# Performance work log

Measured on AMD Instinct MI355X. Metric: run time of the kernel, lower is better.

Reference implementation:

```python
import jax, jax.numpy as jnp
import numpy as np

B, OBS, ACT = 16384, 39, 4
D = 400            # backbone_hidden[-1] == expert_hidden[-1] == task_queries_dim
NE, NT = 8, 10     # num_experts, num_tasks


def setup_inputs() -> dict:
    key = jax.random.key(0)
    ks = jax.random.split(key, 20)
    g = lambda k, shp, fan: jax.random.normal(k, shp, dtype=jnp.float32) / np.sqrt(fan)
    return {
        "obs": jax.random.normal(ks[0], (B, OBS), dtype=jnp.float32),
        "act": jax.random.normal(ks[1], (B, ACT), dtype=jnp.float32),
        "task": jax.random.randint(ks[2], (B,), 0, NT),
        # backbone mlp: [obs+act, 400, 400], relu after each layer
        "bb_w1": g(ks[3], (OBS + ACT, D), OBS + ACT), "bb_b1": jnp.zeros((D,), jnp.float32),
        "bb_w2": g(ks[4], (D, D), D), "bb_b2": jnp.zeros((D,), jnp.float32),
        # 8 expert mlps, stacked: [400 -> 400 -> 400], relu after each layer
        "ex_w1": g(ks[5], (NE, D, D), D), "ex_b1": jnp.zeros((NE, D), jnp.float32),
        "ex_w2": g(ks[6], (NE, D, D), D), "ex_b2": jnp.zeros((NE, D), jnp.float32),
        # attention params
        "key_mat": g(ks[7], (NE, D, D), D),
        "value_mat": g(ks[8], (NE, D, D), D),
        "task_queries": jax.random.normal(ks[9], (NT, D), dtype=jnp.float32),
        # tower mlp: [400, 400, 400, 1], relu on hidden layers, identity output
        "tw_w1": g(ks[10], (D, D), D), "tw_b1": jnp.zeros((D,), jnp.float32),
        "tw_w2": g(ks[11], (D, D), D), "tw_b2": jnp.zeros((D,), jnp.float32),
        "tw_w3": g(ks[12], (D, 1), D), "tw_b3": jnp.zeros((1,), jnp.float32),
    }


def reference(obs, act, task, bb_w1, bb_b1, bb_w2, bb_b2,
              ex_w1, ex_b1, ex_w2, ex_b2,
              key_mat, value_mat, task_queries,
              tw_w1, tw_b1, tw_w2, tw_b2, tw_w3, tw_b3):
    x = jnp.concatenate([obs, act], axis=-1)                       # [B, obs+act]
    h = jax.nn.relu(x @ bb_w1 + bb_b1)
    h = jax.nn.relu(h @ bb_w2 + bb_b2)                             # [B, D]
    # all experts as one batched GEMM: e[n, b, :] = expert_n(h[b])
    e = jax.nn.relu(jnp.einsum('bi,nij->nbj', h, ex_w1) + ex_b1[:, None, :])
    e = jax.nn.relu(jnp.einsum('nbi,nij->nbj', e, ex_w2) + ex_b2[:, None, :])  # [NE, B, D]
    # per-expert key/value projections (einsum 'nij,nj->ni' batched over b)
    vals = jnp.einsum('nij,nbj->bni', value_mat, e)                # [B, NE, D]
    keys = jnp.einsum('nij,nbj->bni', key_mat, e)                  # [B, NE, D]
    q = task_queries[task]                                         # [B, D]
    scores = jnp.einsum('bni,bi->bn', keys, q)                     # [B, NE]
    w = jax.nn.softmax(scores, axis=-1)                            # softmax over experts
    tower_in = jnp.einsum('bn,bni->bi', w, vals)                   # [B, D]
    t = jax.nn.relu(tower_in @ tw_w1 + tw_b1)
    t = jax.nn.relu(t @ tw_w2 + tw_b2)
    qval = t @ tw_w3 + tw_b3                                       # [B, 1]
    return jnp.squeeze(qval, -1)                                   # [B]
```

## Files before the change

kernel.cpp:

```cpp
#include <hip/hip_runtime.h>

typedef _Float16 f16;
typedef f16 f16x8 __attribute__((ext_vector_type(8)));
typedef float f32x4 __attribute__((ext_vector_type(4)));

#define NB 16384
#define D 400
#define DP 416
#define NEXP 8
#define NTASK 10
#define NKT 13

#define MEMFENCE asm volatile("" ::: "memory")
#define BAR() do{ MEMFENCE; __builtin_amdgcn_s_barrier(); MEMFENCE; }while(0)
#define VM(N) asm volatile("s_waitcnt vmcnt(" #N ")" ::: "memory")
#define LGKM0 asm volatile("s_waitcnt lgkmcnt(0)" ::: "memory")

static __device__ __forceinline__ f32x4 mfma16x32(f16x8 a, f16x8 b, f32x4 c){
  return __builtin_amdgcn_mfma_f32_16x16x32_f16(a, b, c, 0, 0, 0);
}
static __device__ __forceinline__ void g2l(const void* g, void* l){
  __builtin_amdgcn_global_load_lds((const __attribute__((address_space(1))) void*)g,
      (__attribute__((address_space(3))) void*)l, 16, 0, 0);
}
static __device__ __forceinline__ f16x8 scale8(f16x8 a, f16 s){
  f16x8 r;
  #pragma unroll
  for (int e=0;e<8;e++) r[e] = a[e]*s;
  return r;
}

static __device__ __forceinline__ void stage_duo(const char* wbase, char* lds, int kt,
                                                 int t0, int dd, int h, int lane){
  const int r = lane >> 3, c = lane & 7, cg = c ^ r;
  g2l(wbase + (size_t)((t0 + dd*2 + (cg>>2))*16 + h*8 + r)*832 + (size_t)kt*64 + (cg&3)*16,
      lds + dd*2048 + h*1024);
}
static __device__ __forceinline__ f16x8 rdB(const f16* buf, int dloc, int t, int lhi, int l15){
  return *(const f16x8*)(buf + dloc*1024 + l15*64 + ((((t*4+lhi) ^ (l15&7)))<<3));
}
static __device__ __forceinline__ f16x8 rdL(const f16* lact, int r, int kt, int lhi){
  int q = kt*4 + lhi;
  int c = (q < 48) ? (q ^ (r&7)) : q;
  return *(const f16x8*)(lact + r*416 + (c<<3));
}
static __device__ __forceinline__ int lact_idx(int r, int col){
  int q = col >> 3;
  int c = (q < 48) ? (q ^ (r&7)) : q;
  return r*416 + (c<<3) + (col&7);
}
static __device__ __forceinline__ void stageB4(const char* wb, char* buf, int kt,
                                               int wv, int lane){
  for (int u = wv; u < 26; u += 4) stage_duo(wb, buf, kt, 0, u>>1, u&1, lane);
}


__global__ void k_build_x(const float* __restrict__ obs, const float* __restrict__ act,
                          f16* __restrict__ x)
{
  int idx = blockIdx.x*256 + threadIdx.x;
  int b = idx >> 6, c = idx & 63;
  float v = 0.f;
  if (c < 39) v = obs[b*39 + c];
  else if (c < 43) v = act[b*4 + (c - 39)];
  x[idx] = (f16)v;
}

__global__ void k_transpose_all(
    const float* __restrict__ bb_w1, const float* __restrict__ bb_w2,
    const float* __restrict__ ex_w1, const float* __restrict__ ex_w2,
    const float* __restrict__ tw_w1, const float* __restrict__ tw_w2,
    f16* __restrict__ bbw1T, f16* __restrict__ bbw2T,
    f16* __restrict__ exw1T, f16* __restrict__ exw2T,
    f16* __restrict__ tw1T,  f16* __restrict__ tw2T)
{
  __shared__ float t[32][33];
  const int z = blockIdx.z;
  const float* in; f16* out; int K = D;
  if (z == 0){ in = bb_w1; out = bbw1T; K = 43; }
  else if (z == 1){ in = bb_w2; out = bbw2T; }
  else if (z < 10){ in = ex_w1 + (size_t)(z-2)*D*D;  out = exw1T + (size_t)(z-2)*DP*DP; }
  else if (z < 18){ in = ex_w2 + (size_t)(z-10)*D*D; out = exw2T + (size_t)(z-10)*DP*DP; }
  else if (z == 18){ in = tw_w1; out = tw1T; }
  else { in = tw_w2; out = tw2T; }
  int tx = threadIdx.x & 31, ty = threadIdx.x >> 5;
  int n0 = blockIdx.x*32, k0 = blockIdx.y*32;
  #pragma unroll
  for (int r=0;r<4;r++){
    int k = k0 + ty + r*8, nn = n0 + tx;
    t[ty + r*8][tx] = (k < K && nn < D) ? in[(size_t)k*D + nn] : 0.f;
  }
  __syncthreads();
  #pragma unroll
  for (int r=0;r<4;r++){
    int nn = n0 + ty + r*8, kp = k0 + tx;
    if (nn < DP && kp < DP) out[(size_t)nn*DP + kp] = (f16)t[tx][ty + r*8];
  }
}

__global__ void k_val_pad(const float* __restrict__ in, f16* __restrict__ out)
{
  int idx = blockIdx.x*256 + threadIdx.x;
  if (idx >= NEXP*DP*DP) return;
  int c = idx % DP, r = (idx / DP) % DP, n = idx / (DP*DP);
  float v = (r < D && c < D) ? in[((size_t)n*D + r)*D + c] : 0.f;
  out[idx] = (f16)v;
}

__global__ void k_kq(const float* __restrict__ key_mat, const float* __restrict__ tq,
                     float* __restrict__ kq)
{
  __shared__ float tqs[NTASK*D];
  int n = blockIdx.x, tid = threadIdx.x;
  for (int i=tid;i<NTASK*D;i+=256) tqs[i] = tq[i];
  __syncthreads();
  float a0[NTASK], a1[NTASK];
  #pragma unroll
  for (int t=0;t<NTASK;t++){ a0[t]=0.f; a1[t]=0.f; }
  const float* km = key_mat + (size_t)n*D*D;
  for (int i=0;i<D;i++){
    float v0 = km[(size_t)i*D + tid];
    float v1 = (tid+256 < D) ? km[(size_t)i*D + tid + 256] : 0.f;
    #pragma unroll
    for (int t=0;t<NTASK;t++){
      float q = tqs[t*D + i];
      a0[t] += v0*q; a1[t] += v1*q;
    }
  }
  #pragma unroll
  for (int t=0;t<NTASK;t++){
    kq[(size_t)n*NTASK*DP + t*DP + tid] = a0[t];
    if (tid+256 < DP) kq[(size_t)n*NTASK*DP + t*DP + tid+256] = (tid+256 < D) ? a1[t] : 0.f;
  }
}


#define MFMA26(a0_, a1_, BUF) do {                                              \
    __builtin_amdgcn_s_setprio(1);                                              \
    _Pragma("unroll")                                                           \
    for (int j=0;j<13;j++){                                                     \
      int tj = ch*13 + j;                                                       \
      f16x8 b = rdB((BUF), tj>>1, tj&1, lhi, l15);                              \
      acc[0][j] = mfma16x32((a0_), b, acc[0][j]);                               \
      acc[1][j] = mfma16x32((a1_), b, acc[1][j]);                               \
    }                                                                           \
    __builtin_amdgcn_s_setprio(0);                                              \
  } while(0)

#define MFMA13(a0_, BUF) do {                                                   \
    __builtin_amdgcn_s_setprio(1);                                              \
    _Pragma("unroll")                                                           \
    for (int j=0;j<13;j++){                                                     \
      int tj = ch*13 + j;                                                       \
      f16x8 b = rdB((BUF), tj>>1, tj&1, lhi, l15);                              \
      acc[j] = mfma16x32((a0_), b, acc[j]);                                     \
    }                                                                           \
    __builtin_amdgcn_s_setprio(0);                                              \
  } while(0)

#define STAGE_W(wb_, buf_, p_, full_) do{                                       \
    int tot_ = (full_) ? 52 : 26;                                               \
    for (int u = wv; u < tot_; u += 4){                                         \
      int kh_ = (u >= 26) ? 1 : 0, uu_ = u - (kh_ ? 26 : 0);                    \
      stage_duo((wb_), (char*)(buf_)[kh_], 2*(p_)+kh_, 0, uu_>>1, uu_&1, lane); \
    }                                                                           \
  } while(0)

__global__ __launch_bounds__(256,2) void k_experts(
    const f16* __restrict__ h16, const f16* __restrict__ w1T, const float* __restrict__ b1s,
    const f16* __restrict__ w2T, const float* __restrict__ b2s,
    f16* __restrict__ e16, const float* __restrict__ kqg, const int* __restrict__ task,
    float* __restrict__ scores)
{
  __shared__ f16 bufB[13*1024];
  __shared__ f16 lact[64*416];
  float (*psum)[2] = (float(*)[2])lact;
  const int tid = threadIdx.x, lane = tid & 63, wv = tid >> 6;
  const int l15 = lane & 15, lhi = lane >> 4;
  const int rh = wv >> 1, ch = wv & 1;
  const int n = blockIdx.x;
  const int rowbase = blockIdx.y * 64;
  const f32x4 Z4 = {0,0,0,0};
  f32x4 acc[2][13];

  const char* wb1 = (const char*)(w1T + (size_t)n*DP*DP);
  const char* wb2 = (const char*)(w2T + (size_t)n*DP*DP);
  const f16* Ab = h16 + (size_t)(rowbase + rh*32 + l15)*DP;

  #pragma unroll
  for (int j=0;j<13;j++){ acc[0][j]=Z4; acc[1][j]=Z4; }
  f16x8 a0 = *(const f16x8*)(Ab + lhi*8);
  f16x8 a1 = *(const f16x8*)(Ab + 16*DP + lhi*8);
  stageB4(wb1, (char*)bufB, 0, wv, lane);
  for (int kt=0; kt<NKT; kt++){
    VM(0); BAR();
    MFMA26(a0, a1, bufB);
    BAR();
    if (kt < NKT-1){
      a0 = *(const f16x8*)(Ab + (kt+1)*32 + lhi*8);
      a1 = *(const f16x8*)(Ab + 16*DP + (kt+1)*32 + lhi*8);
      stageB4(wb1, (char*)bufB, kt+1, wv, lane);
    }
  }
  stageB4(wb2, (char*)bufB, 0, wv, lane);
  #pragma unroll
  for (int j=0;j<13;j++){
    int col = (ch*13+j)*16 + l15;
    float bv = (col<D)? b1s[n*D+col] : 0.f;
    #pragma unroll
    for (int ar=0;ar<2;ar++)
      #pragma unroll
      for (int rr=0;rr<4;rr++){
        float v = acc[ar][j][rr] + bv; v = v>0.f?v:0.f;
        lact[lact_idx(rh*32+ar*16+lhi*4+rr, col)] = (f16)v;
      }
  }
  LGKM0;

  #pragma unroll
  for (int j=0;j<13;j++){ acc[0][j]=Z4; acc[1][j]=Z4; }
  for (int kt=0; kt<NKT; kt++){
    VM(0); BAR();
    f16x8 x0 = rdL(lact, rh*32 + l15, kt, lhi);
    f16x8 x1 = rdL(lact, rh*32 + 16 + l15, kt, lhi);
    MFMA26(x0, x1, bufB);
    BAR();
    if (kt < NKT-1) stageB4(wb2, (char*)bufB, kt+1, wv, lane);
  }
  const float* kqp[2][4];
  const float* kqb = kqg + (size_t)n*NTASK*DP;
  #pragma unroll
  for (int ar=0;ar<2;ar++)
    #pragma unroll
    for (int rr=0;rr<4;rr++){
      int grow = rowbase + rh*32 + ar*16 + lhi*4 + rr;
      kqp[ar][rr] = kqb + (size_t)task[grow]*DP;
    }
  float p_[2][4] = {{0,0,0,0},{0,0,0,0}};
  #pragma unroll
  for (int j=0;j<13;j++){
    int col = (ch*13+j)*16 + l15;
    float bv = (col<D)? b2s[n*D+col] : 0.f;
    #pragma unroll
    for (int ar=0;ar<2;ar++)
      #pragma unroll
      for (int rr=0;rr<4;rr++){
        float v = acc[ar][j][rr] + bv; v = v>0.f?v:0.f;
        e16[((size_t)n*NB + rowbase + rh*32+ar*16+lhi*4+rr)*DP + col] = (f16)v;
        p_[ar][rr] += v * kqp[ar][rr][col];
      }
  }
  #pragma unroll
  for (int ar=0;ar<2;ar++)
    #pragma unroll
    for (int rr=0;rr<4;rr++){
      float p = p_[ar][rr];
      p += __shfl_xor(p, 1, 64);
      p += __shfl_xor(p, 2, 64);
      p += __shfl_xor(p, 4, 64);
      p += __shfl_xor(p, 8, 64);
      if (l15 == 0) psum[rh*32+ar*16+lhi*4+rr][ch] = p;
    }
  LGKM0; BAR();
  if (tid < 64) scores[(size_t)(rowbase + tid)*NEXP + n] = psum[tid][0] + psum[tid][1];
}

__global__ __launch_bounds__(256,2) void k_backbone(
    const f16* __restrict__ x, const f16* __restrict__ w1T, const float* __restrict__ b1,
    const f16* __restrict__ w2T, const float* __restrict__ b2, f16* __restrict__ h16)
{
  __shared__ f16 bufB[2][13*1024];
  __shared__ f16 lact[32*416];
  const int tid = threadIdx.x, lane = tid & 63, wv = tid >> 6;
  const int l15 = lane & 15, lhi = lane >> 4;
  const int rh = wv >> 1, ch = wv & 1;
  const int rowbase = blockIdx.x * 32;
  const f32x4 Z4 = {0,0,0,0};
  f32x4 acc[13];

  const f16* Ab = x + (size_t)(rowbase + rh*16 + l15)*64;

  #pragma unroll
  for (int j=0;j<13;j++) acc[j]=Z4;
  STAGE_W((const char*)w1T, bufB, 0, 1);
  f16x8 a0 = *(const f16x8*)(Ab + lhi*8);
  f16x8 a1 = *(const f16x8*)(Ab + 32 + lhi*8);
  VM(0); BAR();
  MFMA13(a0, bufB[0]);
  MFMA13(a1, bufB[1]);
  BAR();
  STAGE_W((const char*)w2T, bufB, 0, 1);
  #pragma unroll
  for (int j=0;j<13;j++){
    int col = (ch*13+j)*16 + l15;
    float bv = (col<D)? b1[col] : 0.f;
    #pragma unroll
    for (int rr=0;rr<4;rr++){
      float v = acc[j][rr] + bv; v = v>0.f?v:0.f;
      lact[lact_idx(rh*16+lhi*4+rr, col)] = (f16)v;
    }
  }
  LGKM0;

  #pragma unroll
  for (int j=0;j<13;j++) acc[j]=Z4;
  for (int p=0; p<7; p++){
    VM(0); BAR();
    f16x8 x0 = rdL(lact, rh*16 + l15, 2*p, lhi);
    MFMA13(x0, bufB[0]);
    if (p < 6){
      f16x8 x1 = rdL(lact, rh*16 + l15, 2*p+1, lhi);
      MFMA13(x1, bufB[1]);
    }
    BAR();
    if (p < 6) STAGE_W((const char*)w2T, bufB, p+1, (p+1)<6);
  }
  #pragma unroll
  for (int j=0;j<13;j++){
    int col = (ch*13+j)*16 + l15;
    float bv = (col<D)? b2[col] : 0.f;
    #pragma unroll
    for (int rr=0;rr<4;rr++){
      float v = acc[j][rr] + bv; v = v>0.f?v:0.f;
      h16[(size_t)(rowbase + rh*16+lhi*4+rr)*DP + col] = (f16)v;
    }
  }
}

__global__ __launch_bounds__(256,2) void k_attn(
    const f16* __restrict__ e16, const f16* __restrict__ valT,
    const float* __restrict__ scores, f16* __restrict__ ti16)
{
  __shared__ f16 buf[2][7*1024];
  __shared__ float wsm[64*NEXP];
  const int tid = threadIdx.x, lane = tid & 63, wv = tid >> 6;
  const int l15 = lane & 15, lhi = lane >> 4;
  const int rg = wv >> 1, cg = wv & 1;
  const int cb = blockIdx.x;
  const int rowbase = blockIdx.y * 64;
  const int nd = cb ? 6 : 7;
  const int ntw = cb ? 6 : 7;
  const int t0 = cb * 14;
  const f32x4 Z4 = {0,0,0,0};
  f32x4 acc[2][7];
  #pragma unroll
  for (int a=0;a<2;a++)
    #pragma unroll
    for (int j=0;j<7;j++) acc[a][j]=Z4;

  if (tid < 64){
    const float* sr = scores + (size_t)(rowbase + tid)*NEXP;
    float s[8]; float m = -1e30f;
    #pragma unroll
    for (int k=0;k<8;k++){ s[k]=sr[k]; m = fmaxf(m, s[k]); }
    float sum = 0.f;
    #pragma unroll
    for (int k=0;k<8;k++){ s[k] = expf(s[k]-m); sum += s[k]; }
    float inv = 1.f/sum;
    #pragma unroll
    for (int k=0;k<8;k++) wsm[tid*NEXP + k] = s[k]*inv;
  }

  #define STAGE_A(n_, p_) do {                                                  \
    const char* vb_ = (const char*)(valT + (size_t)(n_)*DP*DP);                 \
    int nu_ = nd*2, tot_ = ((p_)<6) ? nd*4 : nd*2;                              \
    for (int u = wv; u < tot_; u += 4){                                         \
      int kh_ = (u >= nu_) ? 1 : 0, uu_ = u - (kh_ ? nu_ : 0);                  \
      stage_duo(vb_, (char*)buf[kh_], 2*(p_)+kh_, t0, uu_>>1, uu_&1, lane);     \
    }                                                                           \
  } while(0)

  #define LDA_A(n_, kt_, ar_) \
    (*(const f16x8*)(e16 + ((size_t)(n_)*NB + rowbase + rg*32 + (ar_)*16 + l15)*DP + (kt_)*32 + lhi*8))

  STAGE_A(0, 0);
  f16x8 aC00 = LDA_A(0,0,0), aC01 = LDA_A(0,0,1);
  f16x8 aC10 = LDA_A(0,1,0), aC11 = LDA_A(0,1,1);
  LGKM0;

  for (int n=0;n<NEXP;n++){
    for (int p=0;p<7;p++){
      int s = n*7 + p;
      VM(0); BAR();
      f16 w0 = (f16)wsm[(rg*32      + l15)*NEXP + n];
      f16 w1 = (f16)wsm[(rg*32 + 16 + l15)*NEXP + n];
      {
        f16x8 as0 = scale8(aC00, w0), as1 = scale8(aC01, w1);
        __builtin_amdgcn_s_setprio(1);
        #pragma unroll
        for (int j=0;j<7;j++) if (j<ntw){
          int tl = cg*ntw + j;
          f16x8 b = rdB(buf[0], tl>>1, tl&1, lhi, l15);
          acc[0][j] = mfma16x32(as0, b, acc[0][j]);
          acc[1][j] = mfma16x32(as1, b, acc[1][j]);
        }
        __builtin_amdgcn_s_setprio(0);
      }
      if (p < 6){
        f16x8 as0 = scale8(aC10, w0), as1 = scale8(aC11, w1);
        __builtin_amdgcn_s_setprio(1);
        #pragma unroll
        for (int j=0;j<7;j++) if (j<ntw){
          int tl = cg*ntw + j;
          f16x8 b = rdB(buf[1], tl>>1, tl&1, lhi, l15);
          acc[0][j] = mfma16x32(as0, b, acc[0][j]);
          acc[1][j] = mfma16x32(as1, b, acc[1][j]);
        }
        __builtin_amdgcn_s_setprio(0);
      }
      BAR();
      if (s < NEXP*7 - 1){
        int p2 = (p==6) ? 0 : p+1;
        int n2 = (p==6) ? n+1 : n;
        STAGE_A(n2, p2);
        aC00 = LDA_A(n2, 2*p2,   0); aC01 = LDA_A(n2, 2*p2,   1);
        if (p2 < 6){ aC10 = LDA_A(n2, 2*p2+1, 0); aC11 = LDA_A(n2, 2*p2+1, 1); }
      }
    }
  }
  #pragma unroll
  for (int ar=0;ar<2;ar++)
    #pragma unroll
    for (int j=0;j<7;j++) if (j<ntw){
      int col = (t0 + cg*ntw + j)*16 + l15;
      #pragma unroll
      for (int rr=0;rr<4;rr++)
        ti16[(size_t)(rowbase + rg*32 + ar*16 + lhi*4 + rr)*DP + col] = (f16)acc[ar][j][rr];
    }
}

__global__ __launch_bounds__(256,2) void k_mlp3(
    const f16* __restrict__ ti16,
    const f16* __restrict__ tw1T, const float* __restrict__ tb1,
    const f16* __restrict__ tw2T, const float* __restrict__ tb2,
    const float* __restrict__ tw3, const float* __restrict__ tb3,
    float* __restrict__ out)
{
  __shared__ f16 bufB[2][13*1024];
  __shared__ f16 lact[32*416];
  float (*psum)[2] = (float(*)[2])lact;
  const int tid = threadIdx.x, lane = tid & 63, wv = tid >> 6;
  const int l15 = lane & 15, lhi = lane >> 4;
  const int rh = wv >> 1, ch = wv & 1;
  const int rowbase = blockIdx.x * 32;
  const f32x4 Z4 = {0,0,0,0};
  f32x4 acc[13];

  const f16* Ab = ti16 + (size_t)(rowbase + rh*16 + l15)*DP;

  #pragma unroll
  for (int j=0;j<13;j++) acc[j]=Z4;
  STAGE_W((const char*)tw1T, bufB, 0, 1);
  f16x8 a0 = *(const f16x8*)(Ab + lhi*8);
  f16x8 a1 = *(const f16x8*)(Ab + 32 + lhi*8);
  for (int p=0; p<7; p++){
    VM(0); BAR();
    MFMA13(a0, bufB[0]);
    if (p < 6) MFMA13(a1, bufB[1]);
    BAR();
    if (p < 6){
      STAGE_W((const char*)tw1T, bufB, p+1, (p+1)<6);
      a0 = *(const f16x8*)(Ab + (2*p+2)*32 + lhi*8);
      if (p+1 < 6) a1 = *(const f16x8*)(Ab + (2*p+3)*32 + lhi*8);
    }
  }
  STAGE_W((const char*)tw2T, bufB, 0, 1);
  #pragma unroll
  for (int j=0;j<13;j++){
    int col = (ch*13+j)*16 + l15;
    float bv = (col<D)? tb1[col] : 0.f;
    #pragma unroll
    for (int rr=0;rr<4;rr++){
      float v = acc[j][rr] + bv; v = v>0.f?v:0.f;
      lact[lact_idx(rh*16+lhi*4+rr, col)] = (f16)v;
    }
  }
  LGKM0;

  #pragma unroll
  for (int j=0;j<13;j++) acc[j]=Z4;
  for (int p=0; p<7; p++){
    VM(0); BAR();
    f16x8 x0 = rdL(lact, rh*16 + l15, 2*p, lhi);
    MFMA13(x0, bufB[0]);
    if (p < 6){
      f16x8 x1 = rdL(lact, rh*16 + l15, 2*p+1, lhi);
      MFMA13(x1, bufB[1]);
    }
    BAR();
    if (p < 6) STAGE_W((const char*)tw2T, bufB, p+1, (p+1)<6);
  }
  float p_[4] = {0,0,0,0};
  #pragma unroll
  for (int j=0;j<13;j++){
    int col = (ch*13+j)*16 + l15;
    float bv = (col<D)? tb2[col] : 0.f;
    float w3 = (col<D)? tw3[col] : 0.f;
    #pragma unroll
    for (int rr=0;rr<4;rr++){
      float v = acc[j][rr] + bv; v = v>0.f?v:0.f;
      p_[rr] += v * w3;
    }
  }
  #pragma unroll
  for (int rr=0;rr<4;rr++){
    float p = p_[rr];
    p += __shfl_xor(p, 1, 64);
    p += __shfl_xor(p, 2, 64);
    p += __shfl_xor(p, 4, 64);
    p += __shfl_xor(p, 8, 64);
    if (l15 == 0) psum[rh*16+lhi*4+rr][ch] = p;
  }
  LGKM0; BAR();
  if (tid < 32) out[rowbase + tid] = psum[tid][0] + psum[tid][1] + tb3[0];
}


extern "C" void kernel_launch(void* const* d_in, const int* in_sizes, int n_in,
                              void* d_out, int out_size, void* d_ws, size_t ws_size,
                              hipStream_t stream)
{
  const float* obs     = (const float*)d_in[0];
  const float* act     = (const float*)d_in[1];
  const int*   task    = (const int*)  d_in[2];
  const float* bb_w1   = (const float*)d_in[3];
  const float* bb_b1   = (const float*)d_in[4];
  const float* bb_w2   = (const float*)d_in[5];
  const float* bb_b2   = (const float*)d_in[6];
  const float* ex_w1   = (const float*)d_in[7];
  const float* ex_b1   = (const float*)d_in[8];
  const float* ex_w2   = (const float*)d_in[9];
  const float* ex_b2   = (const float*)d_in[10];
  const float* key_mat = (const float*)d_in[11];
  const float* val_mat = (const float*)d_in[12];
  const float* tq      = (const float*)d_in[13];
  const float* tw_w1   = (const float*)d_in[14];
  const float* tw_b1   = (const float*)d_in[15];
  const float* tw_w2   = (const float*)d_in[16];
  const float* tw_b2   = (const float*)d_in[17];
  const float* tw_w3   = (const float*)d_in[18];
  const float* tw_b3   = (const float*)d_in[19];

  char* ws = (char*)d_ws;
  size_t off = 0;
  auto alloc = [&](size_t bytes){ void* p = ws + off; off += (bytes + 255) & ~(size_t)255; return p; };
  f16*   x16   = (f16*)  alloc((size_t)NB*64*2);
  f16*   h16   = (f16*)  alloc((size_t)NB*DP*2);
  f16*   e16   = (f16*)  alloc((size_t)NEXP*NB*DP*2);
  f16*   ti16  = (f16*)  alloc((size_t)NB*DP*2);
  float* scors = (float*)alloc((size_t)NB*NEXP*4);
  float* kq    = (float*)alloc((size_t)NEXP*NTASK*DP*4);
  f16*   bbw1T = (f16*)  alloc((size_t)DP*DP*2);
  f16*   bbw2T = (f16*)  alloc((size_t)DP*DP*2);
  f16*   exw1T = (f16*)  alloc((size_t)NEXP*DP*DP*2);
  f16*   exw2T = (f16*)  alloc((size_t)NEXP*DP*DP*2);
  f16*   valT  = (f16*)  alloc((size_t)NEXP*DP*DP*2);
  f16*   tw1T  = (f16*)  alloc((size_t)DP*DP*2);
  f16*   tw2T  = (f16*)  alloc((size_t)DP*DP*2);
  (void)ws_size; (void)in_sizes; (void)n_in; (void)out_size;

  k_build_x<<<NB*64/256, 256, 0, stream>>>(obs, act, x16);
  k_transpose_all<<<dim3(13,13,20), 256, 0, stream>>>(
      bb_w1, bb_w2, ex_w1, ex_w2, tw_w1, tw_w2,
      bbw1T, bbw2T, exw1T, exw2T, tw1T, tw2T);
  k_val_pad<<<(NEXP*DP*DP + 255)/256, 256, 0, stream>>>(val_mat, valT);
  k_kq<<<NEXP, 256, 0, stream>>>(key_mat, tq, kq);

  k_backbone<<<NB/32, 256, 0, stream>>>(x16, bbw1T, bb_b1, bbw2T, bb_b2, h16);
  k_experts<<<dim3(NEXP, NB/64), 256, 0, stream>>>(h16, exw1T, ex_b1, exw2T, ex_b2,
                                                   e16, kq, task, scors);
  k_attn<<<dim3(2, NB/64), 256, 0, stream>>>(e16, valT, scors, ti16);
  k_mlp3<<<NB/32, 256, 0, stream>>>(ti16, tw1T, tw_b1, tw2T, tw_b2, tw_w3, tw_b3,
                                    (float*)d_out);
}
```

Measured before the change: 400.5 us.

## Enlarge expert kernel tile to 128 rows with 512 threads and two k-steps per barrier

```diff
diff --git a/kernel.cpp b/kernel.cpp
--- a/kernel.cpp
+++ b/kernel.cpp
@@ -48,10 +48,6 @@
   int q = col >> 3;
   int c = (q < 48) ? (q ^ (r&7)) : q;
   return r*416 + (c<<3) + (col&7);
-}
-static __device__ __forceinline__ void stageB4(const char* wb, char* buf, int kt,
-                                               int wv, int lane){
-  for (int u = wv; u < 26; u += 4) stage_duo(wb, buf, kt, 0, u>>1, u&1, lane);
 }
 
 
@@ -166,20 +162,28 @@
     }                                                                           \
   } while(0)
 
-__global__ __launch_bounds__(256,2) void k_experts(
+#define STAGE_W8(wb_, buf_, p_, full_) do{                                      \
+    int tot_ = (full_) ? 52 : 26;                                               \
+    for (int u = wv; u < tot_; u += 8){                                         \
+      int kh_ = (u >= 26) ? 1 : 0, uu_ = u - (kh_ ? 26 : 0);                    \
+      stage_duo((wb_), (char*)(buf_)[kh_], 2*(p_)+kh_, 0, uu_>>1, uu_&1, lane); \
+    }                                                                           \
+  } while(0)
+
+__global__ __launch_bounds__(512,2) void k_experts(
     const f16* __restrict__ h16, const f16* __restrict__ w1T, const float* __restrict__ b1s,
     const f16* __restrict__ w2T, const float* __restrict__ b2s,
     f16* __restrict__ e16, const float* __restrict__ kqg, const int* __restrict__ task,
     float* __restrict__ scores)
 {
-  __shared__ f16 bufB[13*1024];
-  __shared__ f16 lact[64*416];
+  __shared__ f16 bufB[2][13*1024];
+  __shared__ f16 lact[128*416];
   float (*psum)[2] = (float(*)[2])lact;
   const int tid = threadIdx.x, lane = tid & 63, wv = tid >> 6;
   const int l15 = lane & 15, lhi = lane >> 4;
   const int rh = wv >> 1, ch = wv & 1;
   const int n = blockIdx.x;
-  const int rowbase = blockIdx.y * 64;
+  const int rowbase = blockIdx.y * 128;
   const f32x4 Z4 = {0,0,0,0};
   f32x4 acc[2][13];
 
@@ -189,20 +193,27 @@
 
   #pragma unroll
   for (int j=0;j<13;j++){ acc[0][j]=Z4; acc[1][j]=Z4; }
-  f16x8 a0 = *(const f16x8*)(Ab + lhi*8);
-  f16x8 a1 = *(const f16x8*)(Ab + 16*DP + lhi*8);
-  stageB4(wb1, (char*)bufB, 0, wv, lane);
-  for (int kt=0; kt<NKT; kt++){
+  STAGE_W8(wb1, bufB, 0, 1);
+  f16x8 a00 = *(const f16x8*)(Ab + lhi*8);
+  f16x8 a01 = *(const f16x8*)(Ab + 16*DP + lhi*8);
+  f16x8 a10 = *(const f16x8*)(Ab + 32 + lhi*8);
+  f16x8 a11 = *(const f16x8*)(Ab + 16*DP + 32 + lhi*8);
+  for (int p=0; p<7; p++){
     VM(0); BAR();
-    MFMA26(a0, a1, bufB);
+    MFMA26(a00, a01, bufB[0]);
+    if (p < 6) MFMA26(a10, a11, bufB[1]);
     BAR();
-    if (kt < NKT-1){
-      a0 = *(const f16x8*)(Ab + (kt+1)*32 + lhi*8);
-      a1 = *(const f16x8*)(Ab + 16*DP + (kt+1)*32 + lhi*8);
-      stageB4(wb1, (char*)bufB, kt+1, wv, lane);
-    }
-  }
-  stageB4(wb2, (char*)bufB, 0, wv, lane);
+    if (p < 6){
+      STAGE_W8(wb1, bufB, p+1, (p+1)<6);
+      a00 = *(const f16x8*)(Ab + (2*p+2)*32 + lhi*8);
+      a01 = *(const f16x8*)(Ab + 16*DP + (2*p+2)*32 + lhi*8);
+      if (p+1 < 6){
+        a10 = *(const f16x8*)(Ab + (2*p+3)*32 + lhi*8);
+        a11 = *(const f16x8*)(Ab + 16*DP + (2*p+3)*32 + lhi*8);
+      }
+    }
+  }
+  STAGE_W8(wb2, bufB, 0, 1);
   #pragma unroll
   for (int j=0;j<13;j++){
     int col = (ch*13+j)*16 + l15;
@@ -219,13 +230,20 @@
 
   #pragma unroll
   for (int j=0;j<13;j++){ acc[0][j]=Z4; acc[1][j]=Z4; }
-  for (int kt=0; kt<NKT; kt++){
+  for (int p=0; p<7; p++){
     VM(0); BAR();
-    f16x8 x0 = rdL(lact, rh*32 + l15, kt, lhi);
-    f16x8 x1 = rdL(lact, rh*32 + 16 + l15, kt, lhi);
-    MFMA26(x0, x1, bufB);
+    {
+      f16x8 x0 = rdL(lact, rh*32 + l15, 2*p, lhi);
+      f16x8 x1 = rdL(lact, rh*32 + 16 + l15, 2*p, lhi);
+      MFMA26(x0, x1, bufB[0]);
+    }
+    if (p < 6){
+      f16x8 x0 = rdL(lact, rh*32 + l15, 2*p+1, lhi);
+      f16x8 x1 = rdL(lact, rh*32 + 16 + l15, 2*p+1, lhi);
+      MFMA26(x0, x1, bufB[1]);
+    }
     BAR();
-    if (kt < NKT-1) stageB4(wb2, (char*)bufB, kt+1, wv, lane);
+    if (p < 6) STAGE_W8(wb2, bufB, p+1, (p+1)<6);
   }
   const float* kqp[2][4];
   const float* kqb = kqg + (size_t)n*NTASK*DP;
@@ -262,7 +280,7 @@
       if (l15 == 0) psum[rh*32+ar*16+lhi*4+rr][ch] = p;
     }
   LGKM0; BAR();
-  if (tid < 64) scores[(size_t)(rowbase + tid)*NEXP + n] = psum[tid][0] + psum[tid][1];
+  if (tid < 128) scores[(size_t)(rowbase + tid)*NEXP + n] = psum[tid][0] + psum[tid][1];
 }
 
 __global__ __launch_bounds__(256,2) void k_backbone(
@@ -567,8 +585,8 @@
   k_kq<<<NEXP, 256, 0, stream>>>(key_mat, tq, kq);
 
   k_backbone<<<NB/32, 256, 0, stream>>>(x16, bbw1T, bb_b1, bbw2T, bb_b2, h16);
-  k_experts<<<dim3(NEXP, NB/64), 256, 0, stream>>>(h16, exw1T, ex_b1, exw2T, ex_b2,
-                                                   e16, kq, task, scors);
+  k_experts<<<dim3(NEXP, NB/128), 512, 0, stream>>>(h16, exw1T, ex_b1, exw2T, ex_b2,
+                                                    e16, kq, task, scors);
   k_attn<<<dim3(2, NB/64), 256, 0, stream>>>(e16, valT, scors, ti16);
   k_mlp3<<<NB/32, 256, 0, stream>>>(ti16, tw1T, tw_b1, tw2T, tw_b2, tw_w3, tw_b3,
                                     (float*)d_out);
```

Result: no change. 407.1 us (+1.7%).

## Spill expert hidden layer to global memory and parallelize key-query precompute

Applied to the files above, without the earlier changes.

```diff
diff --git a/kernel.cpp b/kernel.cpp
--- a/kernel.cpp
+++ b/kernel.cpp
@@ -110,27 +110,28 @@
 __global__ void k_kq(const float* __restrict__ key_mat, const float* __restrict__ tq,
                      float* __restrict__ kq)
 {
+  __shared__ float kcol[D*32];
   __shared__ float tqs[NTASK*D];
-  int n = blockIdx.x, tid = threadIdx.x;
-  for (int i=tid;i<NTASK*D;i+=256) tqs[i] = tq[i];
+  const int n = blockIdx.x, cb = blockIdx.y, tid = threadIdx.x;
+  const int c0 = cb*32;
+  const float* km = key_mat + (size_t)n*D*D;
+  for (int idx=tid; idx<NTASK*D; idx+=256) tqs[idx] = tq[idx];
+  for (int idx=tid; idx<D*32; idx+=256){
+    int i = idx>>5, c = idx&31;
+    int col = c0 + c;
+    kcol[idx] = (col < D) ? km[(size_t)i*D + col] : 0.f;
+  }
   __syncthreads();
-  float a0[NTASK], a1[NTASK];
-  #pragma unroll
-  for (int t=0;t<NTASK;t++){ a0[t]=0.f; a1[t]=0.f; }
-  const float* km = key_mat + (size_t)n*D*D;
-  for (int i=0;i<D;i++){
-    float v0 = km[(size_t)i*D + tid];
-    float v1 = (tid+256 < D) ? km[(size_t)i*D + tid + 256] : 0.f;
-    #pragma unroll
-    for (int t=0;t<NTASK;t++){
-      float q = tqs[t*D + i];
-      a0[t] += v0*q; a1[t] += v1*q;
-    }
-  }
-  #pragma unroll
-  for (int t=0;t<NTASK;t++){
-    kq[(size_t)n*NTASK*DP + t*DP + tid] = a0[t];
-    if (tid+256 < DP) kq[(size_t)n*NTASK*DP + t*DP + tid+256] = (tid+256 < D) ? a1[t] : 0.f;
+  const int c = tid & 31, tg = tid >> 5;
+  #pragma unroll
+  for (int rep=0; rep<2; rep++){
+    int t = tg + rep*8;
+    if (t < NTASK){
+      float acc = 0.f;
+      for (int i=0;i<D;i++) acc += kcol[i*32+c] * tqs[t*D+i];
+      int col = c0 + c;
+      if (col < DP) kq[((size_t)n*NTASK + t)*DP + col] = acc;
+    }
   }
 }
 
@@ -166,15 +167,14 @@
     }                                                                           \
   } while(0)
 
-__global__ __launch_bounds__(256,2) void k_experts(
+__global__ __launch_bounds__(256,4) void k_experts(
     const f16* __restrict__ h16, const f16* __restrict__ w1T, const float* __restrict__ b1s,
     const f16* __restrict__ w2T, const float* __restrict__ b2s,
     f16* __restrict__ e16, const float* __restrict__ kqg, const int* __restrict__ task,
     float* __restrict__ scores)
 {
   __shared__ f16 bufB[13*1024];
-  __shared__ f16 lact[64*416];
-  float (*psum)[2] = (float(*)[2])lact;
+  __shared__ float psum[64][2];
   const int tid = threadIdx.x, lane = tid & 63, wv = tid >> 6;
   const int l15 = lane & 15, lhi = lane >> 4;
   const int rh = wv >> 1, ch = wv & 1;
@@ -185,20 +185,22 @@
 
   const char* wb1 = (const char*)(w1T + (size_t)n*DP*DP);
   const char* wb2 = (const char*)(w2T + (size_t)n*DP*DP);
-  const f16* Ab = h16 + (size_t)(rowbase + rh*32 + l15)*DP;
+  const f16* Ab1 = h16 + (size_t)(rowbase + rh*32 + l15)*DP;
+  f16* Eb = e16 + ((size_t)n*NB + rowbase)*DP;
+  const f16* Ab2 = Eb + (size_t)(rh*32 + l15)*DP;
 
   #pragma unroll
   for (int j=0;j<13;j++){ acc[0][j]=Z4; acc[1][j]=Z4; }
-  f16x8 a0 = *(const f16x8*)(Ab + lhi*8);
-  f16x8 a1 = *(const f16x8*)(Ab + 16*DP + lhi*8);
+  f16x8 a0 = *(const f16x8*)(Ab1 + lhi*8);
+  f16x8 a1 = *(const f16x8*)(Ab1 + 16*DP + lhi*8);
   stageB4(wb1, (char*)bufB, 0, wv, lane);
   for (int kt=0; kt<NKT; kt++){
     VM(0); BAR();
     MFMA26(a0, a1, bufB);
     BAR();
     if (kt < NKT-1){
-      a0 = *(const f16x8*)(Ab + (kt+1)*32 + lhi*8);
-      a1 = *(const f16x8*)(Ab + 16*DP + (kt+1)*32 + lhi*8);
+      a0 = *(const f16x8*)(Ab1 + (kt+1)*32 + lhi*8);
+      a1 = *(const f16x8*)(Ab1 + 16*DP + (kt+1)*32 + lhi*8);
       stageB4(wb1, (char*)bufB, kt+1, wv, lane);
     }
   }
@@ -212,20 +214,24 @@
       #pragma unroll
       for (int rr=0;rr<4;rr++){
         float v = acc[ar][j][rr] + bv; v = v>0.f?v:0.f;
-        lact[lact_idx(rh*32+ar*16+lhi*4+rr, col)] = (f16)v;
+        Eb[(size_t)(rh*32+ar*16+lhi*4+rr)*DP + col] = (f16)v;
       }
   }
-  LGKM0;
+  VM(0); BAR();
 
   #pragma unroll
   for (int j=0;j<13;j++){ acc[0][j]=Z4; acc[1][j]=Z4; }
+  a0 = *(const f16x8*)(Ab2 + lhi*8);
+  a1 = *(const f16x8*)(Ab2 + 16*DP + lhi*8);
   for (int kt=0; kt<NKT; kt++){
     VM(0); BAR();
-    f16x8 x0 = rdL(lact, rh*32 + l15, kt, lhi);
-    f16x8 x1 = rdL(lact, rh*32 + 16 + l15, kt, lhi);
-    MFMA26(x0, x1, bufB);
+    MFMA26(a0, a1, bufB);
     BAR();
-    if (kt < NKT-1) stageB4(wb2, (char*)bufB, kt+1, wv, lane);
+    if (kt < NKT-1){
+      a0 = *(const f16x8*)(Ab2 + (kt+1)*32 + lhi*8);
+      a1 = *(const f16x8*)(Ab2 + 16*DP + (kt+1)*32 + lhi*8);
+      stageB4(wb2, (char*)bufB, kt+1, wv, lane);
+    }
   }
   const float* kqp[2][4];
   const float* kqb = kqg + (size_t)n*NTASK*DP;
@@ -246,7 +252,7 @@
       #pragma unroll
       for (int rr=0;rr<4;rr++){
         float v = acc[ar][j][rr] + bv; v = v>0.f?v:0.f;
-        e16[((size_t)n*NB + rowbase + rh*32+ar*16+lhi*4+rr)*DP + col] = (f16)v;
+        Eb[(size_t)(rh*32+ar*16+lhi*4+rr)*DP + col] = (f16)v;
         p_[ar][rr] += v * kqp[ar][rr][col];
       }
   }
@@ -564,7 +570,7 @@
       bb_w1, bb_w2, ex_w1, ex_w2, tw_w1, tw_w2,
       bbw1T, bbw2T, exw1T, exw2T, tw1T, tw2T);
   k_val_pad<<<(NEXP*DP*DP + 255)/256, 256, 0, stream>>>(val_mat, valT);
-  k_kq<<<NEXP, 256, 0, stream>>>(key_mat, tq, kq);
+  k_kq<<<dim3(NEXP, 13), 256, 0, stream>>>(key_mat, tq, kq);
 
   k_backbone<<<NB/32, 256, 0, stream>>>(x16, bbw1T, bb_b1, bbw2T, bb_b2, h16);
   k_experts<<<dim3(NEXP, NB/64), 256, 0, stream>>>(h16, exw1T, ex_b1, exw2T, ex_b2,
```

After: 1.022 ms. 2.55x slower.
